# Performance work log

Hardware: AMD Instinct MI355X
Metric: run time of the kernel (lower is better)

## Reference

```python
import jax, jax.numpy as jnp
import numpy as np

T, B, L = 40, 64, 80
D_IN = 256
H = 4 * D_IN  # 1024
A = 18


def _lstm_scan(x, h0, c0, W_ih, W_hh, b_ih, b_hh):
    # x: [S,B,in] -> outputs [S,B,H]; PyTorch gate order i,f,g,o
    b = b_ih + b_hh
    def step(carry, xt):
        h, c = carry
        g = xt @ W_ih.T + h @ W_hh.T + b
        i, f, gg, o = jnp.split(g, 4, axis=-1)
        c = jax.nn.sigmoid(f) * c + jax.nn.sigmoid(i) * jnp.tanh(gg)
        h = jax.nn.sigmoid(o) * jnp.tanh(c)
        return (h, c), h
    (h, c), ys = jax.lax.scan(step, (h0, c0), x)
    return ys, h, c


def setup_inputs() -> dict:
    key = jax.random.key(0)
    ks = jax.random.split(key, 24)
    def rn(k, shape, scale=0.02):
        return jax.random.normal(k, shape, dtype=jnp.float32) * scale
    return {
        "state": rn(ks[0], (T, B, D_IN), 1.0),
        "demonstration": rn(ks[1], (T, B, L, D_IN), 1.0),
        "demonstration_length": jax.random.randint(ks[2], (T, B), 1, L + 1, dtype=jnp.int32),
        "h0": jnp.zeros((B, H), jnp.float32),
        "c0": jnp.zeros((B, H), jnp.float32),
        "enc_Wih": rn(ks[3], (4 * H, D_IN)),
        "enc_Whh": rn(ks[4], (4 * H, H)),
        "enc_bih": rn(ks[5], (4 * H,)),
        "enc_bhh": rn(ks[6], (4 * H,)),
        "attn_W": rn(ks[7], (1, 2 * H)),
        "attn_b": rn(ks[8], (1,)),
        "comb_W": rn(ks[9], (H, H + D_IN)),
        "comb_b": rn(ks[10], (H,)),
        "lstm_Wih": rn(ks[11], (4 * H, H)),
        "lstm_Whh": rn(ks[12], (4 * H, H)),
        "lstm_bih": rn(ks[13], (4 * H,)),
        "lstm_bhh": rn(ks[14], (4 * H,)),
        "mid_W": rn(ks[15], (H, H)),
        "mid_b": rn(ks[16], (H,)),
        "out_W": rn(ks[17], (A, H)),
        "out_b": rn(ks[18], (A,)),
    }


def reference(state, demonstration, demonstration_length, h0, c0,
              enc_Wih, enc_Whh, enc_bih, enc_bhh,
              attn_W, attn_b, comb_W, comb_b,
              lstm_Wih, lstm_Whh, lstm_bih, lstm_bhh,
              mid_W, mid_b, out_W, out_b):
    lengths = demonstration_length[0]              # [B], only t=0 lengths used (as in original)
    demo0 = demonstration[0]                       # [B,L,D_IN], only t=0 demo used
    z = jnp.zeros((B, H), demo0.dtype)
    enc, _, _ = _lstm_scan(demo0.transpose(1, 0, 2), z, z,
                           enc_Wih, enc_Whh, enc_bih, enc_bhh)  # [L,B,H]
    enc = enc.transpose(1, 0, 2)                   # [B,L,H]
    mask = jnp.arange(L)[None, :] < lengths[:, None]  # [B,L]
    # attn(cat(enc, h)) == enc @ Wd^T + h @ Wh^T + b (split of the concat linear)
    Wd, Wh = attn_W[:, :H], attn_W[:, H:]          # [1,H] each
    score_d = (enc @ Wd.T)[..., 0] + attn_b[0]     # [B,L], constant over t
    lstm_b = lstm_bih + lstm_bhh

    def step(carry, obs_t):
        h, c = carry
        scores = score_d + h @ Wh.T                # [B,L] ([B,1] broadcast)
        scores = jnp.where(mask, scores, -jnp.inf)
        w = jax.nn.softmax(scores, axis=-1)        # masked softmax over demo steps
        attn_applied = jnp.einsum('bl,blh->bh', w, enc)
        x = jax.nn.relu(jnp.concatenate([attn_applied, obs_t], axis=-1) @ comb_W.T + comb_b)
        g = x @ lstm_Wih.T + h @ lstm_Whh.T + lstm_b
        i, f, gg, o = jnp.split(g, 4, axis=-1)
        c = jax.nn.sigmoid(f) * c + jax.nn.sigmoid(i) * jnp.tanh(gg)
        h = jax.nn.sigmoid(o) * jnp.tanh(c)
        m = h @ mid_W.T + mid_b                    # no activation between middle and output (as in source)
        q_t = m @ out_W.T + out_b
        return (h, c), q_t

    (h, c), q = jax.lax.scan(step, (h0, c0), state)  # q: [T,B,A]
    return q, h, c
```

## Files before the change

### kernel.cpp

```cpp
#include <hip/hip_runtime.h>
#include <hip/hip_bf16.h>

#define TT 40
#define BB 64
#define LL 80
#define DD 256
#define HH 1024
#define G4H 4096
#define AA 18
#define KENC 1280
#define KLSTM 2048
#define KCOMB 1280
#define NB 256
#define NT 512
#define QSZ (TT*BB*AA)

typedef __bf16 bf16x8 __attribute__((ext_vector_type(8)));
typedef float  f32x4  __attribute__((ext_vector_type(4)));

#define OFF_WENC   ((size_t)0)
#define OFF_WLSTM  (OFF_WENC  + (size_t)G4H*KENC*2)
#define OFF_WCOMB  (OFF_WLSTM + (size_t)G4H*KLSTM*2)
#define OFF_WMID   (OFF_WCOMB + (size_t)HH*KCOMB*2)
#define OFF_BIASE  (OFF_WMID  + (size_t)HH*HH*2)
#define OFF_BIASL  (OFF_BIASE + (size_t)G4H*4)
#define OFF_DEMO   (OFF_BIASL + (size_t)G4H*4)
#define OFF_STATE  (OFF_DEMO  + (size_t)BB*LL*DD*2)
#define OFF_ENC    (OFF_STATE + (size_t)TT*BB*DD*2)
#define OFF_HDEC   (OFF_ENC   + (size_t)BB*LL*HH*2)
#define OFF_XALL   (OFF_HDEC  + (size_t)TT*BB*HH*2)
#define OFF_MF     (OFF_XALL  + (size_t)TT*BB*HH*2)
#define OFF_ATTNS  (OFF_MF    + (size_t)TT*BB*HH*2)
#define OFF_HROT   (OFF_ATTNS + (size_t)BB*HH*2)
#define NSLOT_E    81
#define NSLOT_D    41
#define OFF_BAR    (OFF_HROT  + (size_t)(NSLOT_E+NSLOT_D)*BB*HH*2)
#define FLAG_STRIDE 16
#define BAR_BYTES  (NB*FLAG_STRIDE*4)

__device__ __forceinline__ float sigm(float x){ return 1.f/(1.f+__expf(-x)); }

__device__ __forceinline__ float wred_sum(float v){
#pragma unroll
  for (int s=32; s>0; s>>=1) v += __shfl_xor(v, s, 64);
  return v;
}
__device__ __forceinline__ float wred_max(float v){
#pragma unroll
  for (int s=32; s>0; s>>=1) v = fmaxf(v, __shfl_xor(v, s, 64));
  return v;
}

__device__ __forceinline__ unsigned pack_bf16(float a, float b){
  unsigned short ua = __builtin_bit_cast(unsigned short, (__bf16)a);
  unsigned short ub = __builtin_bit_cast(unsigned short, (__bf16)b);
  return (unsigned)ua | ((unsigned)ub << 16);
}

__device__ __forceinline__ void st_u32_sc(unsigned* p, unsigned v){
  __hip_atomic_store(p, v, __ATOMIC_RELAXED, __HIP_MEMORY_SCOPE_AGENT);
}
__device__ __forceinline__ void st_b16_sc(__bf16* p, float v){
  unsigned short u = __builtin_bit_cast(unsigned short, (__bf16)v);
  asm volatile("global_store_short %0, %1, off sc0 sc1"
               :: "v"(p), "v"((unsigned)u) : "memory");
}

__device__ __forceinline__ void gbar_arrive(unsigned* flags, unsigned target, int bk){
  __syncthreads();
  if (threadIdx.x == 0) {
    __builtin_amdgcn_fence(__ATOMIC_RELEASE, "agent");
    __hip_atomic_store(flags + (size_t)bk*FLAG_STRIDE, target,
                       __ATOMIC_RELAXED, __HIP_MEMORY_SCOPE_AGENT);
  }
}
__device__ __forceinline__ void gbar_wait(unsigned* flags, unsigned target){
  if (threadIdx.x < 64) {
    unsigned long long spins = 0;
    for (;;) {
      unsigned a0 = __hip_atomic_load(flags + (size_t)threadIdx.x*FLAG_STRIDE,       __ATOMIC_RELAXED, __HIP_MEMORY_SCOPE_AGENT);
      unsigned a1 = __hip_atomic_load(flags + (size_t)(64+threadIdx.x)*FLAG_STRIDE,  __ATOMIC_RELAXED, __HIP_MEMORY_SCOPE_AGENT);
      unsigned a2 = __hip_atomic_load(flags + (size_t)(128+threadIdx.x)*FLAG_STRIDE, __ATOMIC_RELAXED, __HIP_MEMORY_SCOPE_AGENT);
      unsigned a3 = __hip_atomic_load(flags + (size_t)(192+threadIdx.x)*FLAG_STRIDE, __ATOMIC_RELAXED, __HIP_MEMORY_SCOPE_AGENT);
      bool ok = (a0 >= target) && (a1 >= target) && (a2 >= target) && (a3 >= target);
      if (__all((int)ok)) break;
      if (++spins > (1ull<<20)) break;
      __builtin_amdgcn_s_sleep(1);
    }
  }
  __syncthreads();
  asm volatile("" ::: "memory");
}

__global__ void k_pack_enc(const float* __restrict__ wih, const float* __restrict__ whh,
                           const float* __restrict__ bih, const float* __restrict__ bhh,
                           __bf16* __restrict__ dst, float* __restrict__ bias){
  int p = blockIdx.x;
  int gate = p & 3, jj = (p >> 2) & 3, bq = p >> 4;
  int orig = gate*HH + bq*4 + jj;
  if (threadIdx.x == 0) bias[p] = bih[orig] + bhh[orig];
  const float* s0 = wih + (size_t)orig*DD;
  const float* s1 = whh + (size_t)orig*HH;
  __bf16* d = dst + (size_t)p*KENC;
  for (int k = threadIdx.x; k < KENC; k += blockDim.x)
    d[k] = (__bf16)(k < DD ? s0[k] : s1[k-DD]);
}
__global__ void k_pack_lstm(const float* __restrict__ wih, const float* __restrict__ whh,
                            const float* __restrict__ bih, const float* __restrict__ bhh,
                            __bf16* __restrict__ dst, float* __restrict__ bias){
  int p = blockIdx.x;
  int gate = p & 3, jj = (p >> 2) & 3, bq = p >> 4;
  int orig = gate*HH + bq*4 + jj;
  if (threadIdx.x == 0) bias[p] = bih[orig] + bhh[orig];
  const float* s0 = wih + (size_t)orig*HH;
  const float* s1 = whh + (size_t)orig*HH;
  __bf16* d = dst + (size_t)p*KLSTM;
  for (int k = threadIdx.x; k < KLSTM; k += blockDim.x)
    d[k] = (__bf16)(k < HH ? s0[k] : s1[k-HH]);
}
__global__ void k_conv(const float* __restrict__ src, __bf16* __restrict__ dst, int n){
  int i = blockIdx.x*blockDim.x + threadIdx.x;
  if (i < n) dst[i] = (__bf16)src[i];
}

__global__ __launch_bounds__(NT, 1)
void k_main(const int* __restrict__ demlen,
            const float* __restrict__ h0, const float* __restrict__ c0,
            const float* __restrict__ attn_w,
            const float* __restrict__ comb_b, const float* __restrict__ mid_b,
            const float* __restrict__ out_w, const float* __restrict__ out_b,
            float* __restrict__ out, char* __restrict__ ws){
  const int bk = blockIdx.x, tid = threadIdx.x;
  const int wv = tid >> 6, ln = tid & 63;
  const int l15 = ln & 15, lhi = ln >> 4;
  const int klane = lhi * 8;
  const int gtid = bk*NT + tid;

  __bf16* wEnc  = (__bf16*)(ws + OFF_WENC);
  __bf16* wLstm = (__bf16*)(ws + OFF_WLSTM);
  __bf16* wComb = (__bf16*)(ws + OFF_WCOMB);
  __bf16* wMid  = (__bf16*)(ws + OFF_WMID);
  const float* bE = (const float*)(ws + OFF_BIASE);
  const float* bL = (const float*)(ws + OFF_BIASL);
  __bf16* demoC = (__bf16*)(ws + OFF_DEMO);
  __bf16* stateB= (__bf16*)(ws + OFF_STATE);
  __bf16* encB  = (__bf16*)(ws + OFF_ENC);
  __bf16* hdec  = (__bf16*)(ws + OFF_HDEC);
  __bf16* xall  = (__bf16*)(ws + OFF_XALL);
  __bf16* mf    = (__bf16*)(ws + OFF_MF);
  __bf16* attnS = (__bf16*)(ws + OFF_ATTNS);
  __bf16* hrotE = (__bf16*)(ws + OFF_HROT);
  __bf16* hrotD = hrotE + (size_t)NSLOT_E*BB*HH;
  unsigned* flags = (unsigned*)(ws + OFF_BAR);

  __shared__ float g_lds [BB*17];
  __shared__ float g_lds2[BB*17];
  __shared__ float sc_sh[LL];
  __shared__ float w_sh[LL];

  unsigned bar = 0;
  const int m_ = tid >> 1, q2 = tid & 1;
  const int j0_ = bk*4 + 2*q2;
  const int mt = wv & 3;
  const int am = mt*16 + l15;
  const int khalf = wv >> 2;

  float cfa = 0.f, cfb = 0.f;

  for (int i = gtid; i < BB*HH/2; i += NB*NT) st_u32_sc((unsigned*)hrotE + i, 0u);
  ++bar; gbar_arrive(flags, bar, bk);

  for (int t = 0; t < LL; ++t) {
    gbar_wait(flags, bar);
    const __bf16* hR = hrotE + (size_t)t*BB*HH;
    const __bf16* brow = wEnc + (size_t)(bk*16 + l15)*KENC;
    const int kbase = khalf * 640;

    f32x4 acc = {0.f,0.f,0.f,0.f};
#pragma unroll 8
    for (int kk = 0; kk < 640; kk += 32) {
      int k0 = kbase + kk + klane;
      const __bf16* pa = (k0 < DD) ? demoC + ((size_t)am*LL + t)*DD + k0
                                   : hR + (size_t)am*HH + (k0 - DD);
      acc = __builtin_amdgcn_mfma_f32_16x16x32_bf16(*(const bf16x8*)pa,
                                                    *(const bf16x8*)(brow + k0), acc, 0,0,0);
    }
    {
      float* gl = khalf ? g_lds2 : g_lds;
      int r0 = mt*16 + lhi*4;
#pragma unroll
      for (int r = 0; r < 4; ++r) gl[(r0+r)*17 + l15] = acc[r];
    }
    __syncthreads();
    if (tid < 128) {
      char* hWg = (char*)(hrotE + (size_t)(t+1)*BB*HH);
      int gb = m_*17 + q2*8, cb = bk*16 + q2*8;
      float gi0 = g_lds[gb+0]+g_lds2[gb+0]+bE[cb+0], gf0 = g_lds[gb+1]+g_lds2[gb+1]+bE[cb+1];
      float gg0 = g_lds[gb+2]+g_lds2[gb+2]+bE[cb+2], go0 = g_lds[gb+3]+g_lds2[gb+3]+bE[cb+3];
      float gi1 = g_lds[gb+4]+g_lds2[gb+4]+bE[cb+4], gf1 = g_lds[gb+5]+g_lds2[gb+5]+bE[cb+5];
      float gg1 = g_lds[gb+6]+g_lds2[gb+6]+bE[cb+6], go1 = g_lds[gb+7]+g_lds2[gb+7]+bE[cb+7];
      float cn0 = sigm(gf0)*cfa + sigm(gi0)*tanhf(gg0);
      float cn1 = sigm(gf1)*cfb + sigm(gi1)*tanhf(gg1);
      float hn0 = sigm(go0)*tanhf(cn0);
      float hn1 = sigm(go1)*tanhf(cn1);
      cfa = cn0; cfb = cn1;
      unsigned hp = pack_bf16(hn0, hn1);
      st_u32_sc((unsigned*)(hWg + m_*2048 + j0_*2), hp);
      st_u32_sc((unsigned*)(encB + ((size_t)m_*LL + t)*HH + j0_), hp);
    }
    ++bar; gbar_arrive(flags, bar, bk);
  }

  gbar_wait(flags, bar);
  {
    int b = bk >> 2, qq = bk & 3;
    for (int i = 0; i < 10; ++i) {
      int l = wv*10 + i;
      const __bf16* er = encB + ((size_t)b*LL + l)*HH + ln*16;
      bf16x8 e0 = *(const bf16x8*)(er);
      bf16x8 e1 = *(const bf16x8*)(er + 8);
      float part = 0.f;
#pragma unroll
      for (int j = 0; j < 8; ++j) {
        part += (float)e0[j] * attn_w[ln*16 + j];
        part += (float)e1[j] * attn_w[ln*16 + 8 + j];
      }
      part = wred_sum(part);
      if (ln == 0) sc_sh[l] = part;
    }
    __syncthreads();
    if (wv == 0) {
      int len = demlen[b];
      float s0 = (ln < len) ? sc_sh[ln] : -1e30f;
      float s1 = (ln < 16 && 64+ln < len) ? sc_sh[64+ln] : -1e30f;
      float mx = wred_max(fmaxf(s0, s1));
      float e0 = __expf(s0 - mx);
      float e1 = (ln < 16) ? __expf(s1 - mx) : 0.f;
      float inv = 1.f / wred_sum(e0 + e1);
      w_sh[ln] = e0 * inv;
      if (ln < 16) w_sh[64+ln] = e1 * inv;
    }
    __syncthreads();
    if (tid < 256) {
      int col = qq*256 + tid;
      float a = 0.f;
      const __bf16* eb = encB + (size_t)b*LL*HH + col;
#pragma unroll 4
      for (int l = 0; l < LL; ++l) a += w_sh[l] * (float)eb[(size_t)l*HH];
      st_b16_sc(attnS + (size_t)b*HH + col, a);
    }
    for (int i = gtid; i < BB*HH/2; i += NB*NT) {
      int i2 = i*2;
      st_u32_sc((unsigned*)hrotD + i, pack_bf16(h0[i2], h0[i2+1]));
    }
    if (tid < 128) {
      cfa = c0[m_*HH + j0_];
      cfb = c0[m_*HH + j0_ + 1];
    }
  }
  ++bar; gbar_arrive(flags, bar, bk);

  gbar_wait(flags, bar);
  {
    int g = bk*8 + wv;
    for (int i = 0; i < 5; ++i) {
      int ti = i*2048 + g;
      int mtt = ti >> 6, nt = ti & 63;
      f32x4 acc = {0.f,0.f,0.f,0.f};
      const __bf16* brow = wComb + (size_t)(nt*16 + l15)*KCOMB;
      int r = mtt*16 + l15, bb = r & 63;
      const __bf16* aat = attnS + (size_t)bb*HH;
      const __bf16* ast = stateB + (size_t)r*DD;
#pragma unroll 8
      for (int kk = 0; kk < KCOMB; kk += 32) {
        int k0 = kk + klane;
        bf16x8 af = (k0 < HH) ? *(const bf16x8*)(aat + k0)
                              : *(const bf16x8*)(ast + (k0-HH));
        acc = __builtin_amdgcn_mfma_f32_16x16x32_bf16(af, *(const bf16x8*)(brow + k0), acc, 0,0,0);
      }
      int col = nt*16 + l15;
      float cb = comb_b[col];
      int r0 = mtt*16 + lhi*4;
#pragma unroll
      for (int rr = 0; rr < 4; ++rr)
        st_b16_sc(xall + (size_t)(r0+rr)*HH + col, fmaxf(acc[rr]+cb, 0.f));
    }
  }
  ++bar; gbar_arrive(flags, bar, bk);

  for (int t = 0; t < TT; ++t) {
    gbar_wait(flags, bar);
    const __bf16* hR = hrotD + (size_t)t*BB*HH;
    const __bf16* brow = wLstm + (size_t)(bk*16 + l15)*KLSTM;
    const int kbase = khalf * HH;
    const __bf16* arow = khalf ? (hR + (size_t)am*HH)
                               : (xall + ((size_t)t*BB + am)*HH);

    f32x4 acc = {0.f,0.f,0.f,0.f};
#pragma unroll 8
    for (int kk = 0; kk < HH; kk += 32) {
      int k0 = kk + klane;
      acc = __builtin_amdgcn_mfma_f32_16x16x32_bf16(*(const bf16x8*)(arow + k0),
                                                    *(const bf16x8*)(brow + kbase + k0), acc, 0,0,0);
    }
    {
      float* gl = khalf ? g_lds2 : g_lds;
      int r0 = mt*16 + lhi*4;
#pragma unroll
      for (int r = 0; r < 4; ++r) gl[(r0+r)*17 + l15] = acc[r];
    }
    __syncthreads();
    if (tid < 128) {
      char* hWg = (char*)(hrotD + (size_t)(t+1)*BB*HH);
      int gb = m_*17 + q2*8, cb = bk*16 + q2*8;
      float gi0 = g_lds[gb+0]+g_lds2[gb+0]+bL[cb+0], gf0 = g_lds[gb+1]+g_lds2[gb+1]+bL[cb+1];
      float gg0 = g_lds[gb+2]+g_lds2[gb+2]+bL[cb+2], go0 = g_lds[gb+3]+g_lds2[gb+3]+bL[cb+3];
      float gi1 = g_lds[gb+4]+g_lds2[gb+4]+bL[cb+4], gf1 = g_lds[gb+5]+g_lds2[gb+5]+bL[cb+5];
      float gg1 = g_lds[gb+6]+g_lds2[gb+6]+bL[cb+6], go1 = g_lds[gb+7]+g_lds2[gb+7]+bL[cb+7];
      float cn0 = sigm(gf0)*cfa + sigm(gi0)*tanhf(gg0);
      float cn1 = sigm(gf1)*cfb + sigm(gi1)*tanhf(gg1);
      float hn0 = sigm(go0)*tanhf(cn0);
      float hn1 = sigm(go1)*tanhf(cn1);
      cfa = cn0; cfb = cn1;
      unsigned hp = pack_bf16(hn0, hn1);
      st_u32_sc((unsigned*)(hWg + m_*2048 + j0_*2), hp);
      st_u32_sc((unsigned*)(hdec + ((size_t)t*BB + m_)*HH + j0_), hp);
      if (t == TT-1) {
        out[QSZ + m_*HH + j0_]     = hn0;
        out[QSZ + m_*HH + j0_ + 1] = hn1;
      }
    }
    ++bar; gbar_arrive(flags, bar, bk);
  }

  if (tid < 128) {
    out[QSZ + BB*HH + m_*HH + j0_]     = cfa;
    out[QSZ + BB*HH + m_*HH + j0_ + 1] = cfb;
  }

  gbar_wait(flags, bar);
  {
    int g = bk*8 + wv;
    for (int i = 0; i < 5; ++i) {
      int ti = i*2048 + g;
      int mtt = ti >> 6, nt = ti & 63;
      f32x4 acc = {0.f,0.f,0.f,0.f};
      const __bf16* brow = wMid + (size_t)(nt*16 + l15)*HH;
      const __bf16* arow2 = hdec + (size_t)(mtt*16 + l15)*HH;
#pragma unroll 8
      for (int kk = 0; kk < HH; kk += 32) {
        int k0 = kk + klane;
        acc = __builtin_amdgcn_mfma_f32_16x16x32_bf16(*(const bf16x8*)(arow2 + k0),
                                                      *(const bf16x8*)(brow + k0), acc, 0,0,0);
      }
      int col = nt*16 + l15;
      float mb = mid_b[col];
      int r0 = mtt*16 + lhi*4;
#pragma unroll
      for (int rr = 0; rr < 4; ++rr)
        st_b16_sc(mf + (size_t)(r0+rr)*HH + col, acc[rr]+mb);
    }
  }
  ++bar; gbar_arrive(flags, bar, bk);

  gbar_wait(flags, bar);
  {
    int g = bk*8 + wv;
    for (int i = 0; i < 2; ++i) {
      int row = i*2048 + g;
      if (row < TT*BB) {
        const __bf16* mr = mf + (size_t)row*HH;
        float mreg[16];
#pragma unroll
        for (int k = 0; k < 16; ++k) mreg[k] = (float)mr[ln + 64*k];
        for (int a = 0; a < AA; ++a) {
          float p = 0.f;
#pragma unroll
          for (int k = 0; k < 16; ++k) p += mreg[k] * out_w[(size_t)a*HH + ln + 64*k];
          p = wred_sum(p);
          if (ln == 0) out[(size_t)row*AA + a] = p + out_b[a];
        }
      }
    }
  }
}

extern "C" void kernel_launch(void* const* d_in, const int* in_sizes, int n_in,
                              void* d_out, int out_size, void* d_ws, size_t ws_size,
                              hipStream_t stream) {
  (void)in_sizes; (void)n_in; (void)out_size; (void)ws_size;
  const float* state    = (const float*)d_in[0];
  const float* demo     = (const float*)d_in[1];
  const int*   demlen   = (const int*)d_in[2];
  const float* h0       = (const float*)d_in[3];
  const float* c0       = (const float*)d_in[4];
  const float* enc_wih  = (const float*)d_in[5];
  const float* enc_whh  = (const float*)d_in[6];
  const float* enc_bih  = (const float*)d_in[7];
  const float* enc_bhh  = (const float*)d_in[8];
  const float* attn_w   = (const float*)d_in[9];
  const float* comb_w   = (const float*)d_in[11];
  const float* comb_b   = (const float*)d_in[12];
  const float* lstm_wih = (const float*)d_in[13];
  const float* lstm_whh = (const float*)d_in[14];
  const float* lstm_bih = (const float*)d_in[15];
  const float* lstm_bhh = (const float*)d_in[16];
  const float* mid_w    = (const float*)d_in[17];
  const float* mid_b    = (const float*)d_in[18];
  const float* out_w    = (const float*)d_in[19];
  const float* out_b    = (const float*)d_in[20];
  char* ws = (char*)d_ws;

  (void)hipMemsetAsync(ws + OFF_BAR, 0, BAR_BYTES, stream);
  k_pack_enc <<<G4H, 256, 0, stream>>>(enc_wih, enc_whh, enc_bih, enc_bhh,
                                       (__bf16*)(ws + OFF_WENC), (float*)(ws + OFF_BIASE));
  k_pack_lstm<<<G4H, 256, 0, stream>>>(lstm_wih, lstm_whh, lstm_bih, lstm_bhh,
                                       (__bf16*)(ws + OFF_WLSTM), (float*)(ws + OFF_BIASL));
  k_conv<<<(HH*KCOMB + 255)/256, 256, 0, stream>>>(comb_w, (__bf16*)(ws + OFF_WCOMB), HH*KCOMB);
  k_conv<<<(HH*HH   + 255)/256, 256, 0, stream>>>(mid_w,  (__bf16*)(ws + OFF_WMID),  HH*HH);
  k_conv<<<(BB*LL*DD + 255)/256, 256, 0, stream>>>(demo,  (__bf16*)(ws + OFF_DEMO),  BB*LL*DD);
  k_conv<<<(TT*BB*DD + 255)/256, 256, 0, stream>>>(state, (__bf16*)(ws + OFF_STATE), TT*BB*DD);
  k_main<<<NB, NT, 0, stream>>>(demlen, h0, c0, attn_w, comb_b, mid_b,
                                out_w, out_b, (float*)d_out, ws);
}
```

Before: 2.125 ms.

## Double main-kernel threads to split recurrent K into quarters, fuse prep kernels

New measurement: 2.220 ms. 1.04x slower.

```diff
diff --git a/kernel.cpp b/kernel.cpp
--- a/kernel.cpp
+++ b/kernel.cpp
@@ -12,7 +12,7 @@
 #define KLSTM 2048
 #define KCOMB 1280
 #define NB 256
-#define NT 512
+#define NT 1024
 #define QSZ (TT*BB*AA)
 
 typedef __bf16 bf16x8 __attribute__((ext_vector_type(8)));
@@ -50,7 +50,6 @@
   for (int s=32; s>0; s>>=1) v = fmaxf(v, __shfl_xor(v, s, 64));
   return v;
 }
-
 __device__ __forceinline__ unsigned pack_bf16(float a, float b){
   unsigned short ua = __builtin_bit_cast(unsigned short, (__bf16)a);
   unsigned short ub = __builtin_bit_cast(unsigned short, (__bf16)b);
@@ -92,35 +91,58 @@
   asm volatile("" ::: "memory");
 }
 
-__global__ void k_pack_enc(const float* __restrict__ wih, const float* __restrict__ whh,
-                           const float* __restrict__ bih, const float* __restrict__ bhh,
-                           __bf16* __restrict__ dst, float* __restrict__ bias){
-  int p = blockIdx.x;
-  int gate = p & 3, jj = (p >> 2) & 3, bq = p >> 4;
-  int orig = gate*HH + bq*4 + jj;
-  if (threadIdx.x == 0) bias[p] = bih[orig] + bhh[orig];
-  const float* s0 = wih + (size_t)orig*DD;
-  const float* s1 = whh + (size_t)orig*HH;
-  __bf16* d = dst + (size_t)p*KENC;
-  for (int k = threadIdx.x; k < KENC; k += blockDim.x)
-    d[k] = (__bf16)(k < DD ? s0[k] : s1[k-DD]);
-}
-__global__ void k_pack_lstm(const float* __restrict__ wih, const float* __restrict__ whh,
-                            const float* __restrict__ bih, const float* __restrict__ bhh,
-                            __bf16* __restrict__ dst, float* __restrict__ bias){
-  int p = blockIdx.x;
-  int gate = p & 3, jj = (p >> 2) & 3, bq = p >> 4;
-  int orig = gate*HH + bq*4 + jj;
-  if (threadIdx.x == 0) bias[p] = bih[orig] + bhh[orig];
-  const float* s0 = wih + (size_t)orig*HH;
-  const float* s1 = whh + (size_t)orig*HH;
-  __bf16* d = dst + (size_t)p*KLSTM;
-  for (int k = threadIdx.x; k < KLSTM; k += blockDim.x)
-    d[k] = (__bf16)(k < HH ? s0[k] : s1[k-HH]);
-}
-__global__ void k_conv(const float* __restrict__ src, __bf16* __restrict__ dst, int n){
-  int i = blockIdx.x*blockDim.x + threadIdx.x;
-  if (i < n) dst[i] = (__bf16)src[i];
+#define PB1 4096
+#define PB2 8192
+#define PB3 13312
+#define PB4 17408
+#define PB5 22528
+#define PB6 25088
+#define PGRID 25104
+__global__ __launch_bounds__(256)
+void k_prep(const float* __restrict__ enc_wih, const float* __restrict__ enc_whh,
+            const float* __restrict__ enc_bih, const float* __restrict__ enc_bhh,
+            const float* __restrict__ lstm_wih, const float* __restrict__ lstm_whh,
+            const float* __restrict__ lstm_bih, const float* __restrict__ lstm_bhh,
+            const float* __restrict__ comb_w, const float* __restrict__ mid_w,
+            const float* __restrict__ demo, const float* __restrict__ state,
+            char* __restrict__ ws){
+  int blk = blockIdx.x, tid = threadIdx.x;
+  if (blk < PB1) {
+    int p = blk;
+    int gate = p & 3, jj = (p >> 2) & 3, bq = p >> 4;
+    int orig = gate*HH + bq*4 + jj;
+    if (tid == 0) ((float*)(ws + OFF_BIASE))[p] = enc_bih[orig] + enc_bhh[orig];
+    const float* s0 = enc_wih + (size_t)orig*DD;
+    const float* s1 = enc_whh + (size_t)orig*HH;
+    __bf16* d = (__bf16*)(ws + OFF_WENC) + (size_t)p*KENC;
+    for (int k = tid; k < KENC; k += 256)
+      d[k] = (__bf16)(k < DD ? s0[k] : s1[k-DD]);
+  } else if (blk < PB2) {
+    int p = blk - PB1;
+    int gate = p & 3, jj = (p >> 2) & 3, bq = p >> 4;
+    int orig = gate*HH + bq*4 + jj;
+    if (tid == 0) ((float*)(ws + OFF_BIASL))[p] = lstm_bih[orig] + lstm_bhh[orig];
+    const float* s0 = lstm_wih + (size_t)orig*HH;
+    const float* s1 = lstm_whh + (size_t)orig*HH;
+    __bf16* d = (__bf16*)(ws + OFF_WLSTM) + (size_t)p*KLSTM;
+    for (int k = tid; k < KLSTM; k += 256)
+      d[k] = (__bf16)(k < HH ? s0[k] : s1[k-HH]);
+  } else if (blk < PB3) {
+    int i = (blk - PB2)*256 + tid;
+    ((__bf16*)(ws + OFF_WCOMB))[i] = (__bf16)comb_w[i];
+  } else if (blk < PB4) {
+    int i = (blk - PB3)*256 + tid;
+    ((__bf16*)(ws + OFF_WMID))[i] = (__bf16)mid_w[i];
+  } else if (blk < PB5) {
+    int i = (blk - PB4)*256 + tid;
+    ((__bf16*)(ws + OFF_DEMO))[i] = (__bf16)demo[i];
+  } else if (blk < PB6) {
+    int i = (blk - PB5)*256 + tid;
+    ((__bf16*)(ws + OFF_STATE))[i] = (__bf16)state[i];
+  } else {
+    int i = (blk - PB6)*256 + tid;
+    ((unsigned*)(ws + OFF_BAR))[i] = 0u;
+  }
 }
 
 __global__ __launch_bounds__(NT, 1)
@@ -153,17 +175,18 @@
   __bf16* hrotD = hrotE + (size_t)NSLOT_E*BB*HH;
   unsigned* flags = (unsigned*)(ws + OFF_BAR);
 
-  __shared__ float g_lds [BB*17];
-  __shared__ float g_lds2[BB*17];
+  __shared__ float g_lds[4][BB*17];
   __shared__ float sc_sh[LL];
   __shared__ float w_sh[LL];
 
   unsigned bar = 0;
   const int m_ = tid >> 1, q2 = tid & 1;
   const int j0_ = bk*4 + 2*q2;
-  const int mt = wv & 3;
+  const int mt = wv & 3, kq = wv >> 2;
   const int am = mt*16 + l15;
-  const int khalf = wv >> 2;
+  const int stag = bk >> 3;
+  const int rotE = stag % 10;
+  const int rotD = stag & 15;
 
   float cfa = 0.f, cfb = 0.f;
 
@@ -174,35 +197,35 @@
     gbar_wait(flags, bar);
     const __bf16* hR = hrotE + (size_t)t*BB*HH;
     const __bf16* brow = wEnc + (size_t)(bk*16 + l15)*KENC;
-    const int kbase = khalf * 640;
+    const __bf16* arow = demoC + ((size_t)am*LL + t)*DD;
+    const __bf16* hrow = hR + (size_t)am*HH;
 
     f32x4 acc = {0.f,0.f,0.f,0.f};
-#pragma unroll 8
-    for (int kk = 0; kk < 640; kk += 32) {
-      int k0 = kbase + kk + klane;
-      const __bf16* pa = (k0 < DD) ? demoC + ((size_t)am*LL + t)*DD + k0
-                                   : hR + (size_t)am*HH + (k0 - DD);
+#pragma unroll
+    for (int i = 0; i < 10; ++i) {
+      int idx = i + rotE; if (idx >= 10) idx -= 10;
+      int k0 = kq*320 + idx*32 + klane;
+      const __bf16* pa = (k0 < DD) ? (arow + k0) : (hrow + (k0 - DD));
       acc = __builtin_amdgcn_mfma_f32_16x16x32_bf16(*(const bf16x8*)pa,
                                                     *(const bf16x8*)(brow + k0), acc, 0,0,0);
     }
     {
-      float* gl = khalf ? g_lds2 : g_lds;
       int r0 = mt*16 + lhi*4;
 #pragma unroll
-      for (int r = 0; r < 4; ++r) gl[(r0+r)*17 + l15] = acc[r];
+      for (int r = 0; r < 4; ++r) g_lds[kq][(r0+r)*17 + l15] = acc[r];
     }
     __syncthreads();
     if (tid < 128) {
       char* hWg = (char*)(hrotE + (size_t)(t+1)*BB*HH);
       int gb = m_*17 + q2*8, cb = bk*16 + q2*8;
-      float gi0 = g_lds[gb+0]+g_lds2[gb+0]+bE[cb+0], gf0 = g_lds[gb+1]+g_lds2[gb+1]+bE[cb+1];
-      float gg0 = g_lds[gb+2]+g_lds2[gb+2]+bE[cb+2], go0 = g_lds[gb+3]+g_lds2[gb+3]+bE[cb+3];
-      float gi1 = g_lds[gb+4]+g_lds2[gb+4]+bE[cb+4], gf1 = g_lds[gb+5]+g_lds2[gb+5]+bE[cb+5];
-      float gg1 = g_lds[gb+6]+g_lds2[gb+6]+bE[cb+6], go1 = g_lds[gb+7]+g_lds2[gb+7]+bE[cb+7];
-      float cn0 = sigm(gf0)*cfa + sigm(gi0)*tanhf(gg0);
-      float cn1 = sigm(gf1)*cfb + sigm(gi1)*tanhf(gg1);
-      float hn0 = sigm(go0)*tanhf(cn0);
-      float hn1 = sigm(go1)*tanhf(cn1);
+      float g[8];
+#pragma unroll
+      for (int j = 0; j < 8; ++j)
+        g[j] = g_lds[0][gb+j] + g_lds[1][gb+j] + g_lds[2][gb+j] + g_lds[3][gb+j] + bE[cb+j];
+      float cn0 = sigm(g[1])*cfa + sigm(g[0])*tanhf(g[2]);
+      float cn1 = sigm(g[5])*cfb + sigm(g[4])*tanhf(g[6]);
+      float hn0 = sigm(g[3])*tanhf(cn0);
+      float hn1 = sigm(g[7])*tanhf(cn1);
       cfa = cn0; cfb = cn1;
       unsigned hp = pack_bf16(hn0, hn1);
       st_u32_sc((unsigned*)(hWg + m_*2048 + j0_*2), hp);
@@ -214,8 +237,8 @@
   gbar_wait(flags, bar);
   {
     int b = bk >> 2, qq = bk & 3;
-    for (int i = 0; i < 10; ++i) {
-      int l = wv*10 + i;
+    for (int i = 0; i < 5; ++i) {
+      int l = wv*5 + i;
       const __bf16* er = encB + ((size_t)b*LL + l)*HH + ln*16;
       bf16x8 e0 = *(const bf16x8*)(er);
       bf16x8 e1 = *(const bf16x8*)(er + 8);
@@ -262,28 +285,30 @@
 
   gbar_wait(flags, bar);
   {
-    int g = bk*8 + wv;
-    for (int i = 0; i < 5; ++i) {
-      int ti = i*2048 + g;
-      int mtt = ti >> 6, nt = ti & 63;
-      f32x4 acc = {0.f,0.f,0.f,0.f};
-      const __bf16* brow = wComb + (size_t)(nt*16 + l15)*KCOMB;
-      int r = mtt*16 + l15, bb = r & 63;
-      const __bf16* aat = attnS + (size_t)bb*HH;
-      const __bf16* ast = stateB + (size_t)r*DD;
+    int g = bk*16 + wv;
+    for (int i = 0; i < 3; ++i) {
+      int ti = i*4096 + g;
+      if (ti < 10240) {
+        int mtt = ti >> 6, nt = ti & 63;
+        f32x4 acc = {0.f,0.f,0.f,0.f};
+        const __bf16* brow = wComb + (size_t)(nt*16 + l15)*KCOMB;
+        int r = mtt*16 + l15, bb = r & 63;
+        const __bf16* aat = attnS + (size_t)bb*HH;
+        const __bf16* ast = stateB + (size_t)r*DD;
 #pragma unroll 8
-      for (int kk = 0; kk < KCOMB; kk += 32) {
-        int k0 = kk + klane;
-        bf16x8 af = (k0 < HH) ? *(const bf16x8*)(aat + k0)
-                              : *(const bf16x8*)(ast + (k0-HH));
-        acc = __builtin_amdgcn_mfma_f32_16x16x32_bf16(af, *(const bf16x8*)(brow + k0), acc, 0,0,0);
+        for (int kk = 0; kk < KCOMB; kk += 32) {
+          int k0 = kk + klane;
+          bf16x8 af = (k0 < HH) ? *(const bf16x8*)(aat + k0)
+                                : *(const bf16x8*)(ast + (k0-HH));
+          acc = __builtin_amdgcn_mfma_f32_16x16x32_bf16(af, *(const bf16x8*)(brow + k0), acc, 0,0,0);
+        }
+        int col = nt*16 + l15;
+        float cb = comb_b[col];
+        int r0 = mtt*16 + lhi*4;
+#pragma unroll
+        for (int rr = 0; rr < 4; ++rr)
+          st_b16_sc(xall + (size_t)(r0+rr)*HH + col, fmaxf(acc[rr]+cb, 0.f));
       }
-      int col = nt*16 + l15;
-      float cb = comb_b[col];
-      int r0 = mtt*16 + lhi*4;
-#pragma unroll
-      for (int rr = 0; rr < 4; ++rr)
-        st_b16_sc(xall + (size_t)(r0+rr)*HH + col, fmaxf(acc[rr]+cb, 0.f));
     }
   }
   ++bar; gbar_arrive(flags, bar, bk);
@@ -292,35 +317,35 @@
     gbar_wait(flags, bar);
     const __bf16* hR = hrotD + (size_t)t*BB*HH;
     const __bf16* brow = wLstm + (size_t)(bk*16 + l15)*KLSTM;
-    const int kbase = khalf * HH;
-    const __bf16* arow = khalf ? (hR + (size_t)am*HH)
-                               : (xall + ((size_t)t*BB + am)*HH);
+    const __bf16* xrow = xall + ((size_t)t*BB + am)*HH;
+    const __bf16* hrow = hR + (size_t)am*HH;
 
     f32x4 acc = {0.f,0.f,0.f,0.f};
-#pragma unroll 8
-    for (int kk = 0; kk < HH; kk += 32) {
-      int k0 = kk + klane;
-      acc = __builtin_amdgcn_mfma_f32_16x16x32_bf16(*(const bf16x8*)(arow + k0),
-                                                    *(const bf16x8*)(brow + kbase + k0), acc, 0,0,0);
+#pragma unroll
+    for (int i = 0; i < 16; ++i) {
+      int idx = (i + rotD) & 15;
+      int k0 = kq*512 + idx*32 + klane;
+      const __bf16* pa = (k0 < HH) ? (xrow + k0) : (hrow + (k0 - HH));
+      acc = __builtin_amdgcn_mfma_f32_16x16x32_bf16(*(const bf16x8*)pa,
+                                                    *(const bf16x8*)(brow + k0), acc, 0,0,0);
     }
     {
-      float* gl = khalf ? g_lds2 : g_lds;
       int r0 = mt*16 + lhi*4;
 #pragma unroll
-      for (int r = 0; r < 4; ++r) gl[(r0+r)*17 + l15] = acc[r];
+      for (int r = 0; r < 4; ++r) g_lds[kq][(r0+r)*17 + l15] = acc[r];
     }
     __syncthreads();
     if (tid < 128) {
       char* hWg = (char*)(hrotD + (size_t)(t+1)*BB*HH);
       int gb = m_*17 + q2*8, cb = bk*16 + q2*8;
-      float gi0 = g_lds[gb+0]+g_lds2[gb+0]+bL[cb+0], gf0 = g_lds[gb+1]+g_lds2[gb+1]+bL[cb+1];
-      float gg0 = g_lds[gb+2]+g_lds2[gb+2]+bL[cb+2], go0 = g_lds[gb+3]+g_lds2[gb+3]+bL[cb+3];
-      float gi1 = g_lds[gb+4]+g_lds2[gb+4]+bL[cb+4], gf1 = g_lds[gb+5]+g_lds2[gb+5]+bL[cb+5];
-      float gg1 = g_lds[gb+6]+g_lds2[gb+6]+bL[cb+6], go1 = g_lds[gb+7]+g_lds2[gb+7]+bL[cb+7];
-      float cn0 = sigm(gf0)*cfa + sigm(gi0)*tanhf(gg0);
-      float cn1 = sigm(gf1)*cfb + sigm(gi1)*tanhf(gg1);
-      float hn0 = sigm(go0)*tanhf(cn0);
-      float hn1 = sigm(go1)*tanhf(cn1);
+      float g[8];
+#pragma unroll
+      for (int j = 0; j < 8; ++j)
+        g[j] = g_lds[0][gb+j] + g_lds[1][gb+j] + g_lds[2][gb+j] + g_lds[3][gb+j] + bL[cb+j];
+      float cn0 = sigm(g[1])*cfa + sigm(g[0])*tanhf(g[2]);
+      float cn1 = sigm(g[5])*cfb + sigm(g[4])*tanhf(g[6]);
+      float hn0 = sigm(g[3])*tanhf(cn0);
+      float hn1 = sigm(g[7])*tanhf(cn1);
       cfa = cn0; cfb = cn1;
       unsigned hp = pack_bf16(hn0, hn1);
       st_u32_sc((unsigned*)(hWg + m_*2048 + j0_*2), hp);
@@ -340,46 +365,45 @@
 
   gbar_wait(flags, bar);
   {
-    int g = bk*8 + wv;
-    for (int i = 0; i < 5; ++i) {
-      int ti = i*2048 + g;
-      int mtt = ti >> 6, nt = ti & 63;
-      f32x4 acc = {0.f,0.f,0.f,0.f};
-      const __bf16* brow = wMid + (size_t)(nt*16 + l15)*HH;
-      const __bf16* arow2 = hdec + (size_t)(mtt*16 + l15)*HH;
+    int g = bk*16 + wv;
+    for (int i = 0; i < 3; ++i) {
+      int ti = i*4096 + g;
+      if (ti < 10240) {
+        int mtt = ti >> 6, nt = ti & 63;
+        f32x4 acc = {0.f,0.f,0.f,0.f};
+        const __bf16* brow = wMid + (size_t)(nt*16 + l15)*HH;
+        const __bf16* arow2 = hdec + (size_t)(mtt*16 + l15)*HH;
 #pragma unroll 8
-      for (int kk = 0; kk < HH; kk += 32) {
-        int k0 = kk + klane;
-        acc = __builtin_amdgcn_mfma_f32_16x16x32_bf16(*(const bf16x8*)(arow2 + k0),
-                                                      *(const bf16x8*)(brow + k0), acc, 0,0,0);
+        for (int kk = 0; kk < HH; kk += 32) {
+          int k0 = kk + klane;
+          acc = __builtin_amdgcn_mfma_f32_16x16x32_bf16(*(const bf16x8*)(arow2 + k0),
+                                                        *(const bf16x8*)(brow + k0), acc, 0,0,0);
+        }
+        int col = nt*16 + l15;
+        float mb = mid_b[col];
+        int r0 = mtt*16 + lhi*4;
+#pragma unroll
+        for (int rr = 0; rr < 4; ++rr)
+          st_b16_sc(mf + (size_t)(r0+rr)*HH + col, acc[rr]+mb);
       }
-      int col = nt*16 + l15;
-      float mb = mid_b[col];
-      int r0 = mtt*16 + lhi*4;
-#pragma unroll
-      for (int rr = 0; rr < 4; ++rr)
-        st_b16_sc(mf + (size_t)(r0+rr)*HH + col, acc[rr]+mb);
     }
   }
   ++bar; gbar_arrive(flags, bar, bk);
 
   gbar_wait(flags, bar);
   {
-    int g = bk*8 + wv;
-    for (int i = 0; i < 2; ++i) {
-      int row = i*2048 + g;
-      if (row < TT*BB) {
-        const __bf16* mr = mf + (size_t)row*HH;
-        float mreg[16];
-#pragma unroll
-        for (int k = 0; k < 16; ++k) mreg[k] = (float)mr[ln + 64*k];
-        for (int a = 0; a < AA; ++a) {
-          float p = 0.f;
-#pragma unroll
-          for (int k = 0; k < 16; ++k) p += mreg[k] * out_w[(size_t)a*HH + ln + 64*k];
-          p = wred_sum(p);
-          if (ln == 0) out[(size_t)row*AA + a] = p + out_b[a];
-        }
+    int row = bk*16 + wv;
+    if (row < TT*BB) {
+      const __bf16* mr = mf + (size_t)row*HH;
+      float mreg[16];
+#pragma unroll
+      for (int k = 0; k < 16; ++k) mreg[k] = (float)mr[ln + 64*k];
+      for (int a = 0; a < AA; ++a) {
+        float p = 0.f;
+#pragma unroll
+        for (int k = 0; k < 16; ++k) p += mreg[k] * out_w[(size_t)a*HH + ln + 64*k];
+        p = wred_sum(p);
+        if (ln == 0) out[(size_t)row*AA + a] = p + out_b[a];
       }
     }
   }
@@ -411,15 +435,9 @@
   const float* out_b    = (const float*)d_in[20];
   char* ws = (char*)d_ws;
 
-  (void)hipMemsetAsync(ws + OFF_BAR, 0, BAR_BYTES, stream);
-  k_pack_enc <<<G4H, 256, 0, stream>>>(enc_wih, enc_whh, enc_bih, enc_bhh,
-                                       (__bf16*)(ws + OFF_WENC), (float*)(ws + OFF_BIASE));
-  k_pack_lstm<<<G4H, 256, 0, stream>>>(lstm_wih, lstm_whh, lstm_bih, lstm_bhh,
-                                       (__bf16*)(ws + OFF_WLSTM), (float*)(ws + OFF_BIASL));
-  k_conv<<<(HH*KCOMB + 255)/256, 256, 0, stream>>>(comb_w, (__bf16*)(ws + OFF_WCOMB), HH*KCOMB);
-  k_conv<<<(HH*HH   + 255)/256, 256, 0, stream>>>(mid_w,  (__bf16*)(ws + OFF_WMID),  HH*HH);
-  k_conv<<<(BB*LL*DD + 255)/256, 256, 0, stream>>>(demo,  (__bf16*)(ws + OFF_DEMO),  BB*LL*DD);
-  k_conv<<<(TT*BB*DD + 255)/256, 256, 0, stream>>>(state, (__bf16*)(ws + OFF_STATE), TT*BB*DD);
+  k_prep<<<PGRID, 256, 0, stream>>>(enc_wih, enc_whh, enc_bih, enc_bhh,
+                                    lstm_wih, lstm_whh, lstm_bih, lstm_bhh,
+                                    comb_w, mid_w, demo, state, ws);
   k_main<<<NB, NT, 0, stream>>>(demlen, h0, c0, attn_w, comb_b, mid_b,
                                 out_w, out_b, (float*)d_out, ws);
 }
```

## Use cooperative grid sync and merge prep kernels into one launch

Applied to the files above, without the earlier changes.

Result: slower. 4.927 ms (+131.8%).

```diff
diff --git a/kernel.cpp b/kernel.cpp
--- a/kernel.cpp
+++ b/kernel.cpp
@@ -1,5 +1,8 @@
 #include <hip/hip_runtime.h>
 #include <hip/hip_bf16.h>
+#include <hip/hip_cooperative_groups.h>
+
+namespace cg = cooperative_groups;
 
 #define TT 40
 #define BB 64
@@ -34,9 +37,6 @@
 #define OFF_HROT   (OFF_ATTNS + (size_t)BB*HH*2)
 #define NSLOT_E    81
 #define NSLOT_D    41
-#define OFF_BAR    (OFF_HROT  + (size_t)(NSLOT_E+NSLOT_D)*BB*HH*2)
-#define FLAG_STRIDE 16
-#define BAR_BYTES  (NB*FLAG_STRIDE*4)
 
 __device__ __forceinline__ float sigm(float x){ return 1.f/(1.f+__expf(-x)); }
 
@@ -50,7 +50,6 @@
   for (int s=32; s>0; s>>=1) v = fmaxf(v, __shfl_xor(v, s, 64));
   return v;
 }
-
 __device__ __forceinline__ unsigned pack_bf16(float a, float b){
   unsigned short ua = __builtin_bit_cast(unsigned short, (__bf16)a);
   unsigned short ub = __builtin_bit_cast(unsigned short, (__bf16)b);
@@ -66,70 +65,64 @@
                :: "v"(p), "v"((unsigned)u) : "memory");
 }
 
-__device__ __forceinline__ void gbar_arrive(unsigned* flags, unsigned target, int bk){
-  __syncthreads();
-  if (threadIdx.x == 0) {
-    __builtin_amdgcn_fence(__ATOMIC_RELEASE, "agent");
-    __hip_atomic_store(flags + (size_t)bk*FLAG_STRIDE, target,
-                       __ATOMIC_RELAXED, __HIP_MEMORY_SCOPE_AGENT);
-  }
-}
-__device__ __forceinline__ void gbar_wait(unsigned* flags, unsigned target){
-  if (threadIdx.x < 64) {
-    unsigned long long spins = 0;
-    for (;;) {
-      unsigned a0 = __hip_atomic_load(flags + (size_t)threadIdx.x*FLAG_STRIDE,       __ATOMIC_RELAXED, __HIP_MEMORY_SCOPE_AGENT);
-      unsigned a1 = __hip_atomic_load(flags + (size_t)(64+threadIdx.x)*FLAG_STRIDE,  __ATOMIC_RELAXED, __HIP_MEMORY_SCOPE_AGENT);
-      unsigned a2 = __hip_atomic_load(flags + (size_t)(128+threadIdx.x)*FLAG_STRIDE, __ATOMIC_RELAXED, __HIP_MEMORY_SCOPE_AGENT);
-      unsigned a3 = __hip_atomic_load(flags + (size_t)(192+threadIdx.x)*FLAG_STRIDE, __ATOMIC_RELAXED, __HIP_MEMORY_SCOPE_AGENT);
-      bool ok = (a0 >= target) && (a1 >= target) && (a2 >= target) && (a3 >= target);
-      if (__all((int)ok)) break;
-      if (++spins > (1ull<<20)) break;
-      __builtin_amdgcn_s_sleep(1);
-    }
-  }
-  __syncthreads();
-  asm volatile("" ::: "memory");
-}
-
-__global__ void k_pack_enc(const float* __restrict__ wih, const float* __restrict__ whh,
-                           const float* __restrict__ bih, const float* __restrict__ bhh,
-                           __bf16* __restrict__ dst, float* __restrict__ bias){
-  int p = blockIdx.x;
-  int gate = p & 3, jj = (p >> 2) & 3, bq = p >> 4;
-  int orig = gate*HH + bq*4 + jj;
-  if (threadIdx.x == 0) bias[p] = bih[orig] + bhh[orig];
-  const float* s0 = wih + (size_t)orig*DD;
-  const float* s1 = whh + (size_t)orig*HH;
-  __bf16* d = dst + (size_t)p*KENC;
-  for (int k = threadIdx.x; k < KENC; k += blockDim.x)
-    d[k] = (__bf16)(k < DD ? s0[k] : s1[k-DD]);
-}
-__global__ void k_pack_lstm(const float* __restrict__ wih, const float* __restrict__ whh,
-                            const float* __restrict__ bih, const float* __restrict__ bhh,
-                            __bf16* __restrict__ dst, float* __restrict__ bias){
-  int p = blockIdx.x;
-  int gate = p & 3, jj = (p >> 2) & 3, bq = p >> 4;
-  int orig = gate*HH + bq*4 + jj;
-  if (threadIdx.x == 0) bias[p] = bih[orig] + bhh[orig];
-  const float* s0 = wih + (size_t)orig*HH;
-  const float* s1 = whh + (size_t)orig*HH;
-  __bf16* d = dst + (size_t)p*KLSTM;
-  for (int k = threadIdx.x; k < KLSTM; k += blockDim.x)
-    d[k] = (__bf16)(k < HH ? s0[k] : s1[k-HH]);
-}
-__global__ void k_conv(const float* __restrict__ src, __bf16* __restrict__ dst, int n){
-  int i = blockIdx.x*blockDim.x + threadIdx.x;
-  if (i < n) dst[i] = (__bf16)src[i];
-}
-
-__global__ __launch_bounds__(NT, 1)
+#define PB1 4096
+#define PB2 8192
+#define PB3 13312
+#define PB4 17408
+#define PB5 22528
+#define PGRID 25088
+__global__ __launch_bounds__(256)
+void k_prep(const float* __restrict__ enc_wih, const float* __restrict__ enc_whh,
+            const float* __restrict__ enc_bih, const float* __restrict__ enc_bhh,
+            const float* __restrict__ lstm_wih, const float* __restrict__ lstm_whh,
+            const float* __restrict__ lstm_bih, const float* __restrict__ lstm_bhh,
+            const float* __restrict__ comb_w, const float* __restrict__ mid_w,
+            const float* __restrict__ demo, const float* __restrict__ state,
+            char* __restrict__ ws){
+  int blk = blockIdx.x, tid = threadIdx.x;
+  if (blk < PB1) {
+    int p = blk;
+    int gate = p & 3, jj = (p >> 2) & 3, bq = p >> 4;
+    int orig = gate*HH + bq*4 + jj;
+    if (tid == 0) ((float*)(ws + OFF_BIASE))[p] = enc_bih[orig] + enc_bhh[orig];
+    const float* s0 = enc_wih + (size_t)orig*DD;
+    const float* s1 = enc_whh + (size_t)orig*HH;
+    __bf16* d = (__bf16*)(ws + OFF_WENC) + (size_t)p*KENC;
+    for (int k = tid; k < KENC; k += 256)
+      d[k] = (__bf16)(k < DD ? s0[k] : s1[k-DD]);
+  } else if (blk < PB2) {
+    int p = blk - PB1;
+    int gate = p & 3, jj = (p >> 2) & 3, bq = p >> 4;
+    int orig = gate*HH + bq*4 + jj;
+    if (tid == 0) ((float*)(ws + OFF_BIASL))[p] = lstm_bih[orig] + lstm_bhh[orig];
+    const float* s0 = lstm_wih + (size_t)orig*HH;
+    const float* s1 = lstm_whh + (size_t)orig*HH;
+    __bf16* d = (__bf16*)(ws + OFF_WLSTM) + (size_t)p*KLSTM;
+    for (int k = tid; k < KLSTM; k += 256)
+      d[k] = (__bf16)(k < HH ? s0[k] : s1[k-HH]);
+  } else if (blk < PB3) {
+    int i = (blk - PB2)*256 + tid;
+    ((__bf16*)(ws + OFF_WCOMB))[i] = (__bf16)comb_w[i];
+  } else if (blk < PB4) {
+    int i = (blk - PB3)*256 + tid;
+    ((__bf16*)(ws + OFF_WMID))[i] = (__bf16)mid_w[i];
+  } else if (blk < PB5) {
+    int i = (blk - PB4)*256 + tid;
+    ((__bf16*)(ws + OFF_DEMO))[i] = (__bf16)demo[i];
+  } else {
+    int i = (blk - PB5)*256 + tid;
+    ((__bf16*)(ws + OFF_STATE))[i] = (__bf16)state[i];
+  }
+}
+
+__global__ __launch_bounds__(NT)
 void k_main(const int* __restrict__ demlen,
             const float* __restrict__ h0, const float* __restrict__ c0,
             const float* __restrict__ attn_w,
             const float* __restrict__ comb_b, const float* __restrict__ mid_b,
             const float* __restrict__ out_w, const float* __restrict__ out_b,
             float* __restrict__ out, char* __restrict__ ws){
+  cg::grid_group grid = cg::this_grid();
   const int bk = blockIdx.x, tid = threadIdx.x;
   const int wv = tid >> 6, ln = tid & 63;
   const int l15 = ln & 15, lhi = ln >> 4;
@@ -151,14 +144,12 @@
   __bf16* attnS = (__bf16*)(ws + OFF_ATTNS);
   __bf16* hrotE = (__bf16*)(ws + OFF_HROT);
   __bf16* hrotD = hrotE + (size_t)NSLOT_E*BB*HH;
-  unsigned* flags = (unsigned*)(ws + OFF_BAR);
 
   __shared__ float g_lds [BB*17];
   __shared__ float g_lds2[BB*17];
   __shared__ float sc_sh[LL];
   __shared__ float w_sh[LL];
 
-  unsigned bar = 0;
   const int m_ = tid >> 1, q2 = tid & 1;
   const int j0_ = bk*4 + 2*q2;
   const int mt = wv & 3;
@@ -168,10 +159,9 @@
   float cfa = 0.f, cfb = 0.f;
 
   for (int i = gtid; i < BB*HH/2; i += NB*NT) st_u32_sc((unsigned*)hrotE + i, 0u);
-  ++bar; gbar_arrive(flags, bar, bk);
+  grid.sync();
 
   for (int t = 0; t < LL; ++t) {
-    gbar_wait(flags, bar);
     const __bf16* hR = hrotE + (size_t)t*BB*HH;
     const __bf16* brow = wEnc + (size_t)(bk*16 + l15)*KENC;
     const int kbase = khalf * 640;
@@ -208,10 +198,9 @@
       st_u32_sc((unsigned*)(hWg + m_*2048 + j0_*2), hp);
       st_u32_sc((unsigned*)(encB + ((size_t)m_*LL + t)*HH + j0_), hp);
     }
-    ++bar; gbar_arrive(flags, bar, bk);
-  }
-
-  gbar_wait(flags, bar);
+    grid.sync();
+  }
+
   {
     int b = bk >> 2, qq = bk & 3;
     for (int i = 0; i < 10; ++i) {
@@ -258,9 +247,8 @@
       cfb = c0[m_*HH + j0_ + 1];
     }
   }
-  ++bar; gbar_arrive(flags, bar, bk);
-
-  gbar_wait(flags, bar);
+  grid.sync();
+
   {
     int g = bk*8 + wv;
     for (int i = 0; i < 5; ++i) {
@@ -286,10 +274,9 @@
         st_b16_sc(xall + (size_t)(r0+rr)*HH + col, fmaxf(acc[rr]+cb, 0.f));
     }
   }
-  ++bar; gbar_arrive(flags, bar, bk);
+  grid.sync();
 
   for (int t = 0; t < TT; ++t) {
-    gbar_wait(flags, bar);
     const __bf16* hR = hrotD + (size_t)t*BB*HH;
     const __bf16* brow = wLstm + (size_t)(bk*16 + l15)*KLSTM;
     const int kbase = khalf * HH;
@@ -330,7 +317,7 @@
         out[QSZ + m_*HH + j0_ + 1] = hn1;
       }
     }
-    ++bar; gbar_arrive(flags, bar, bk);
+    grid.sync();
   }
 
   if (tid < 128) {
@@ -338,7 +325,6 @@
     out[QSZ + BB*HH + m_*HH + j0_ + 1] = cfb;
   }
 
-  gbar_wait(flags, bar);
   {
     int g = bk*8 + wv;
     for (int i = 0; i < 5; ++i) {
@@ -361,9 +347,8 @@
         st_b16_sc(mf + (size_t)(r0+rr)*HH + col, acc[rr]+mb);
     }
   }
-  ++bar; gbar_arrive(flags, bar, bk);
-
-  gbar_wait(flags, bar);
+  grid.sync();
+
   {
     int g = bk*8 + wv;
     for (int i = 0; i < 2; ++i) {
@@ -410,16 +395,17 @@
   const float* out_w    = (const float*)d_in[19];
   const float* out_b    = (const float*)d_in[20];
   char* ws = (char*)d_ws;
-
-  (void)hipMemsetAsync(ws + OFF_BAR, 0, BAR_BYTES, stream);
-  k_pack_enc <<<G4H, 256, 0, stream>>>(enc_wih, enc_whh, enc_bih, enc_bhh,
-                                       (__bf16*)(ws + OFF_WENC), (float*)(ws + OFF_BIASE));
-  k_pack_lstm<<<G4H, 256, 0, stream>>>(lstm_wih, lstm_whh, lstm_bih, lstm_bhh,
-                                       (__bf16*)(ws + OFF_WLSTM), (float*)(ws + OFF_BIASL));
-  k_conv<<<(HH*KCOMB + 255)/256, 256, 0, stream>>>(comb_w, (__bf16*)(ws + OFF_WCOMB), HH*KCOMB);
-  k_conv<<<(HH*HH   + 255)/256, 256, 0, stream>>>(mid_w,  (__bf16*)(ws + OFF_WMID),  HH*HH);
-  k_conv<<<(BB*LL*DD + 255)/256, 256, 0, stream>>>(demo,  (__bf16*)(ws + OFF_DEMO),  BB*LL*DD);
-  k_conv<<<(TT*BB*DD + 255)/256, 256, 0, stream>>>(state, (__bf16*)(ws + OFF_STATE), TT*BB*DD);
-  k_main<<<NB, NT, 0, stream>>>(demlen, h0, c0, attn_w, comb_b, mid_b,
-                                out_w, out_b, (float*)d_out, ws);
-}
+  float* outp = (float*)d_out;
+
+  k_prep<<<PGRID, 256, 0, stream>>>(enc_wih, enc_whh, enc_bih, enc_bhh,
+                                    lstm_wih, lstm_whh, lstm_bih, lstm_bhh,
+                                    comb_w, mid_w, demo, state, ws);
+
+  void* args[] = {
+    (void*)&demlen, (void*)&h0, (void*)&c0, (void*)&attn_w,
+    (void*)&comb_b, (void*)&mid_b, (void*)&out_w, (void*)&out_b,
+    (void*)&outp, (void*)&ws
+  };
+  (void)hipLaunchCooperativeKernel(reinterpret_cast<void*>(k_main),
+                                   dim3(NB), dim3(NT), args, 0, stream);
+}
```
